# Kernel tuning notes

Hardware: AMD Instinct MI355X
Metric: run time of the kernel (lower is better)

## Reference

```python
import jax, jax.numpy as jnp
import numpy as np

NEG_INF = -1e30  # value the original assigns to exactly-zero scores


def setup_inputs() -> dict:
    key = jax.random.key(0)
    kq, kk, kv = jax.random.split(key, 3)
    B, Lq, Lk, d = 16, 4096, 4096, 64
    queries = jax.random.normal(kq, (B, Lq, d), dtype=jnp.float32)
    keys = jax.random.normal(kk, (B, Lk, d), dtype=jnp.float32)
    values = jax.random.normal(kv, (B, Lk, d), dtype=jnp.float32)
    return {"queries": queries, "keys": keys, "values": values}


def reference(queries, keys, values):
    d = queries.shape[-1]
    # [B, Lq, Lk] full score matrix, scaled
    scores = jnp.einsum("bqd,bkd->bqk", queries, keys) / jnp.sqrt(
        jnp.asarray(d, dtype=queries.dtype)
    )
    # zero-score masking: scores[scores == 0] = -1e30
    scores = jnp.where(scores == 0, jnp.asarray(NEG_INF, dtype=scores.dtype), scores)
    attn = jax.nn.softmax(scores, axis=-1)
    # dropout prob is 0.0 -> identity
    return jnp.einsum("bqk,bkd->bqd", attn, values)
```

## Files before the change

### kernel.cpp

```cpp
#include <hip/hip_runtime.h>
#include <hip/hip_bf16.h>
#include <math.h>

typedef __attribute__((ext_vector_type(4))) float f32x4;
typedef __attribute__((ext_vector_type(8))) short s16x8;

#define B_    16
#define L_    4096
#define D_    64
#define QB    64
#define KVB   64
#define NT    (L_ / KVB)

#define QSCALE 0.18033688011112042f
#define THR    8.0f

__device__ __forceinline__ unsigned short f2bf(float x) {
  union { float f; unsigned u; } v; v.f = x;
  unsigned r = v.u + 0x7FFFu + ((v.u >> 16) & 1u);
  return (unsigned short)(r >> 16);
}

__device__ __forceinline__ int swz(int x) {
  return ((x & 7) ^ ((x >> 3) & 7)) << 4;
}

__device__ __forceinline__ void gload_lds16(const void* g, void* l) {
  __builtin_amdgcn_global_load_lds(
      (const __attribute__((address_space(1))) void*)g,
      (__attribute__((address_space(3))) void*)l, 16, 0, 0);
}

__device__ __forceinline__ unsigned cvtpk_bf16(float lo, float hi) {
  unsigned r;
  asm("v_cvt_pk_bf16_f32 %0, %1, %2" : "=v"(r) : "v"(lo), "v"(hi));
  return r;
}

__device__ __forceinline__ void pl32_swap(unsigned& a, unsigned& b) {
#if __has_builtin(__builtin_amdgcn_permlane32_swap)
  auto r = __builtin_amdgcn_permlane32_swap(a, b, false, false);
  a = r[0]; b = r[1];
#else
  asm volatile("v_permlane32_swap_b32 %0, %1" : "+v"(a), "+v"(b));
#endif
}

__device__ __forceinline__ void pl16_swap(unsigned& a, unsigned& b) {
#if __has_builtin(__builtin_amdgcn_permlane16_swap)
  auto r = __builtin_amdgcn_permlane16_swap(a, b, false, false);
  a = r[0]; b = r[1];
#else
  asm volatile("v_permlane16_swap_b32 %0, %1" : "+v"(a), "+v"(b));
#endif
}

__device__ __forceinline__ float fexp2(float x) {
#if __has_builtin(__builtin_amdgcn_exp2f)
  return __builtin_amdgcn_exp2f(x);
#else
  return exp2f(x);
#endif
}

__global__ __launch_bounds__(256) void prep_kv3(
    const float* __restrict__ Kg, const float* __restrict__ Vg,
    unsigned short* __restrict__ Kw, unsigned short* __restrict__ Vw) {
  const int tid = threadIdx.x;
  int blk = blockIdx.x;
  if (blk < B_ * NT) {
    const float* src = Kg + (size_t)blk * (KVB * D_);
    char* dst = (char*)(Kw + (size_t)blk * (KVB * D_));
#pragma unroll
    for (int c = 0; c < 2; ++c) {
      const int ch  = tid + c * 256;
      const int key = ch >> 3;
      const int seg = ch & 7;
      const float* p = src + key * D_ + seg * 8;
      f32x4 x0 = *(const f32x4*)p;
      f32x4 x1 = *(const f32x4*)(p + 4);
      union { s16x8 v; unsigned w[4]; } t_;
      t_.w[0] = cvtpk_bf16(x0[0], x0[1]);
      t_.w[1] = cvtpk_bf16(x0[2], x0[3]);
      t_.w[2] = cvtpk_bf16(x1[0], x1[1]);
      t_.w[3] = cvtpk_bf16(x1[2], x1[3]);
      *(s16x8*)(dst + ((key * 128 + seg * 16) ^ swz(key))) = t_.v;
    }
  } else {
    blk -= B_ * NT;
    const int skey2 = (tid >> 3) * 2;
    const int sdseg = tid & 7;
    const float* vp0 = Vg + ((size_t)blk * KVB + skey2) * D_ + sdseg * 8;
    char* vout = (char*)(Vw + (size_t)blk * (KVB * D_));
    f32x4 v0 = *(const f32x4*)(vp0);
    f32x4 v1 = *(const f32x4*)(vp0 + 4);
    f32x4 v2 = *(const f32x4*)(vp0 + D_);
    f32x4 v3 = *(const f32x4*)(vp0 + D_ + 4);
#pragma unroll
    for (int u = 0; u < 2; ++u) {
#pragma unroll
      for (int i = 0; i < 4; ++i) {
        const int d = sdseg * 8 + u * 4 + i;
        unsigned pk = cvtpk_bf16(u ? v1[i] : v0[i], u ? v3[i] : v2[i]);
        *(unsigned*)(vout + ((d * 128 + skey2 * 2) ^ swz(d))) = pk;
      }
    }
  }
}

__global__ __launch_bounds__(256) void attn_fwd4(
    const float* __restrict__ Qg, const unsigned short* __restrict__ Kw,
    const unsigned short* __restrict__ Vw, float* __restrict__ Og) {
  __shared__ unsigned short Ks[2][KVB * D_];
  __shared__ unsigned short Vs[2][KVB * D_];

  const int tid  = threadIdx.x;
  const int wv   = tid >> 6;
  const int lane = tid & 63;
  const int rl   = lane & 15;
  const int kb   = lane >> 4;
  const int kb4  = kb * 4;

  const int blk = blockIdx.x;
  const int b   = blk >> 6;
  const int qt  = blk & 63;

  const float* qrow_p = Qg + ((size_t)b * L_ + qt * QB + wv * 16 + rl) * D_;
  s16x8 aq[2];
#pragma unroll
  for (int h = 0; h < 2; ++h) {
    const float* p = qrow_p + h * 32 + kb * 8;
    f32x4 x0 = *(const f32x4*)p;
    f32x4 x1 = *(const f32x4*)(p + 4);
    union { s16x8 v; unsigned w[4]; } t_;
    t_.w[0] = cvtpk_bf16(x0[0] * QSCALE, x0[1] * QSCALE);
    t_.w[1] = cvtpk_bf16(x0[2] * QSCALE, x0[3] * QSCALE);
    t_.w[2] = cvtpk_bf16(x1[0] * QSCALE, x1[1] * QSCALE);
    t_.w[3] = cvtpk_bf16(x1[2] * QSCALE, x1[3] * QSCALE);
    aq[h] = t_.v;
  }

  int koffA[4], koffB[4], voffA[4], voffB[4];
#pragma unroll
  for (int t = 0; t < 4; ++t) {
    const int key = t * 16 + rl;
    const int kbase = key * 128 + kb * 16;
    koffA[t] = kbase ^ swz(key);
    koffB[t] = (kbase + 64) ^ swz(key);
    voffA[t] = kbase ^ swz(key);
    voffB[t] = (kbase + 64) ^ swz(key);
  }

  f32x4 oacc[4];
#pragma unroll
  for (int t = 0; t < 4; ++t) oacc[t] = (f32x4){0.f, 0.f, 0.f, 0.f};
  float m_r = -3.0e38f, l_r = 0.f;

  char* ks0 = (char*)(&Ks[0][0]);
  char* vs0 = (char*)(&Vs[0][0]);
  const int woff = wv * 2048 ;
  const char* kt = (const char*)(Kw + (size_t)b * L_ * D_) + woff + lane * 16;
  const char* vt = (const char*)(Vw + (size_t)b * L_ * D_) + woff + lane * 16;

  auto compute = [&](const char* kbase, const char* vbase) {
    f32x4 s[4];
    __builtin_amdgcn_s_setprio(1);
#pragma unroll
    for (int t = 0; t < 4; ++t) {
      s16x8 k0 = *(const s16x8*)(kbase + koffA[t]);
      s16x8 k1 = *(const s16x8*)(kbase + koffB[t]);
      f32x4 acc = (f32x4){0.f, 0.f, 0.f, 0.f};
      acc = __builtin_amdgcn_mfma_f32_16x16x32_bf16(k0, aq[0], acc, 0, 0, 0);
      acc = __builtin_amdgcn_mfma_f32_16x16x32_bf16(k1, aq[1], acc, 0, 0, 0);
      s[t] = acc;
    }
    __builtin_amdgcn_s_setprio(0);

    float a0 = fmaxf(fmaxf(s[0][0], s[0][1]), s[0][2]);
    float a1 = fmaxf(fmaxf(s[0][3], s[1][0]), s[1][1]);
    float a2 = fmaxf(fmaxf(s[1][2], s[1][3]), s[2][0]);
    float a3 = fmaxf(fmaxf(s[2][1], s[2][2]), s[2][3]);
    float a4 = fmaxf(fmaxf(s[3][0], s[3][1]), s[3][2]);
    float mx = fmaxf(fmaxf(fmaxf(a0, a1), fmaxf(a2, a3)),
                     fmaxf(a4, s[3][3]));

    if (__any(mx > m_r + THR)) {
      float rmx = fmaxf(mx, __shfl_xor(mx, 16));
      rmx = fmaxf(rmx, __shfl_xor(rmx, 32));
      const float mn = fmaxf(m_r, rmx);
      const float alpha = fexp2(m_r - mn);
      m_r = mn;
      l_r *= alpha;
      const float b0 = __shfl(alpha, kb4 + 0);
      const float b1 = __shfl(alpha, kb4 + 1);
      const float b2 = __shfl(alpha, kb4 + 2);
      const float b3 = __shfl(alpha, kb4 + 3);
#pragma unroll
      for (int t = 0; t < 4; ++t) {
        oacc[t][0] *= b0; oacc[t][1] *= b1;
        oacc[t][2] *= b2; oacc[t][3] *= b3;
      }
    }

    unsigned Wp[4][2];
    float rs = 0.f;
#pragma unroll
    for (int t = 0; t < 4; ++t) {
      const float e0 = fexp2(s[t][0] - m_r);
      const float e1 = fexp2(s[t][1] - m_r);
      const float e2 = fexp2(s[t][2] - m_r);
      const float e3 = fexp2(s[t][3] - m_r);
      rs += (e0 + e1) + (e2 + e3);
      Wp[t][0] = cvtpk_bf16(e0, e1);
      Wp[t][1] = cvtpk_bf16(e2, e3);
    }
    l_r += rs;

    union { s16x8 v; unsigned w[4]; } AF0, AF1;
    {
      unsigned x = Wp[0][0], y = Wp[1][0];
      pl32_swap(x, y); pl16_swap(x, y);
      AF0.w[0] = x; AF0.w[2] = y;
    }
    {
      unsigned x = Wp[0][1], y = Wp[1][1];
      pl32_swap(x, y); pl16_swap(x, y);
      AF0.w[1] = x; AF0.w[3] = y;
    }
    {
      unsigned x = Wp[2][0], y = Wp[3][0];
      pl32_swap(x, y); pl16_swap(x, y);
      AF1.w[0] = x; AF1.w[2] = y;
    }
    {
      unsigned x = Wp[2][1], y = Wp[3][1];
      pl32_swap(x, y); pl16_swap(x, y);
      AF1.w[1] = x; AF1.w[3] = y;
    }

    __builtin_amdgcn_s_setprio(1);
#pragma unroll
    for (int t = 0; t < 4; ++t) {
      s16x8 bv0 = *(const s16x8*)(vbase + voffA[t]);
      s16x8 bv1 = *(const s16x8*)(vbase + voffB[t]);
      f32x4 acc = oacc[t];
      acc = __builtin_amdgcn_mfma_f32_16x16x32_bf16(AF0.v, bv0, acc, 0, 0, 0);
      acc = __builtin_amdgcn_mfma_f32_16x16x32_bf16(AF1.v, bv1, acc, 0, 0, 0);
      oacc[t] = acc;
    }
    __builtin_amdgcn_s_setprio(0);
  };

  gload_lds16(kt,        ks0 + woff);
  gload_lds16(kt + 1024, ks0 + woff + 1024);
  gload_lds16(vt,        vs0 + woff);
  gload_lds16(vt + 1024, vs0 + woff + 1024);
  kt += 8192; vt += 8192;
  __syncthreads();

  int boff = 0;
  for (int kv = 0; kv < NT - 1; ++kv) {
    const int nb = boff ^ 8192;
    gload_lds16(kt,        ks0 + nb + woff);
    gload_lds16(kt + 1024, ks0 + nb + woff + 1024);
    gload_lds16(vt,        vs0 + nb + woff);
    gload_lds16(vt + 1024, vs0 + nb + woff + 1024);
    kt += 8192; vt += 8192;

    compute(ks0 + boff, vs0 + boff);
    __syncthreads();
    boff = nb;
  }
  compute(ks0 + boff, vs0 + boff);

  float lt = l_r + __shfl_xor(l_r, 16);
  lt += __shfl_xor(lt, 32);
  const float linv = 1.0f / lt;
  const float i0 = __shfl(linv, kb4 + 0);
  const float i1 = __shfl(linv, kb4 + 1);
  const float i2 = __shfl(linv, kb4 + 2);
  const float i3 = __shfl(linv, kb4 + 3);
  float inv[4] = {i0, i1, i2, i3};

  float* op = Og + ((size_t)b * L_ + qt * QB + wv * 16 + kb4) * D_;
#pragma unroll
  for (int j = 0; j < 4; ++j)
#pragma unroll
    for (int t = 0; t < 4; ++t)
      op[(size_t)j * D_ + t * 16 + rl] = oacc[t][j] * inv[j];
}

__global__ __launch_bounds__(256) void attn_fwd_fb(
    const float* __restrict__ Qg, const float* __restrict__ Kg,
    const float* __restrict__ Vg, float* __restrict__ Og) {
  __shared__ unsigned short Ksf[KVB * D_];
  __shared__ unsigned short Vsf[KVB * D_];
  __shared__ unsigned short Psf[4][16 * KVB];

  const int tid  = threadIdx.x;
  const int wv   = tid >> 6;
  const int lane = tid & 63;
  const int rl   = lane & 15;
  const int kb   = lane >> 4;

  const int blk = blockIdx.x;
  const int b   = blk / (L_ / QB);
  const int qt  = blk % (L_ / QB);

  const float* qrow_p = Qg + ((size_t)b * L_ + qt * QB + wv * 16 + rl) * D_;
  s16x8 aq[2];
#pragma unroll
  for (int h = 0; h < 2; ++h) {
    const float* p = qrow_p + h * 32 + kb * 8;
    f32x4 x0 = *(const f32x4*)p;
    f32x4 x1 = *(const f32x4*)(p + 4);
    s16x8 w;
#pragma unroll
    for (int i = 0; i < 4; ++i) {
      w[i]     = (short)f2bf(x0[i] * QSCALE);
      w[i + 4] = (short)f2bf(x1[i] * QSCALE);
    }
    aq[h] = w;
  }

  f32x4 oacc[4];
  float m_r[4], l_r[4];
#pragma unroll
  for (int t = 0; t < 4; ++t) oacc[t] = (f32x4){0.f, 0.f, 0.f, 0.f};
#pragma unroll
  for (int j = 0; j < 4; ++j) { m_r[j] = -3.0e38f; l_r[j] = 0.f; }

  const float* kb_p = Kg + (size_t)b * L_ * D_;
  const float* vb_p = Vg + (size_t)b * L_ * D_;
  const int skey2 = (tid >> 3) * 2;
  const int sdseg = tid & 7;

  char* ksc = (char*)Ksf;
  char* vsc = (char*)Vsf;
  char* psc = (char*)(Psf[wv]);

  for (int kv = 0; kv < L_; kv += KVB) {
    __syncthreads();
    {
      const float* kp0 = kb_p + (size_t)(kv + skey2) * D_ + sdseg * 8;
      const float* vp0 = vb_p + (size_t)(kv + skey2) * D_ + sdseg * 8;
#pragma unroll
      for (int q2 = 0; q2 < 2; ++q2) {
        const int key = skey2 + q2;
        f32x4 a0 = *(const f32x4*)(kp0 + q2 * D_);
        f32x4 a1 = *(const f32x4*)(kp0 + q2 * D_ + 4);
        s16x8 w;
#pragma unroll
        for (int i = 0; i < 4; ++i) {
          w[i]     = (short)f2bf(a0[i]);
          w[i + 4] = (short)f2bf(a1[i]);
        }
        *(s16x8*)(ksc + ((key * 128 + sdseg * 16) ^ swz(key))) = w;
      }
      f32x4 v0 = *(const f32x4*)(vp0);
      f32x4 v1 = *(const f32x4*)(vp0 + 4);
      f32x4 v2 = *(const f32x4*)(vp0 + D_);
      f32x4 v3 = *(const f32x4*)(vp0 + D_ + 4);
#pragma unroll
      for (int u = 0; u < 2; ++u) {
#pragma unroll
        for (int i = 0; i < 4; ++i) {
          const int d = sdseg * 8 + u * 4 + i;
          unsigned lo = (unsigned)f2bf(u ? v1[i] : v0[i]);
          unsigned hi = (unsigned)f2bf(u ? v3[i] : v2[i]);
          *(unsigned*)(vsc + ((d * 128 + skey2 * 2) ^ swz(d))) = lo | (hi << 16);
        }
      }
    }
    __syncthreads();

    f32x4 s[4];
#pragma unroll
    for (int t = 0; t < 4; ++t) {
      const int key  = t * 16 + rl;
      const int base = key * 128 + kb * 16;
      s16x8 b0 = *(const s16x8*)(ksc + ((base)      ^ swz(key)));
      s16x8 b1 = *(const s16x8*)(ksc + ((base + 64) ^ swz(key)));
      f32x4 acc = (f32x4){0.f, 0.f, 0.f, 0.f};
      acc = __builtin_amdgcn_mfma_f32_16x16x32_bf16(aq[0], b0, acc, 0, 0, 0);
      acc = __builtin_amdgcn_mfma_f32_16x16x32_bf16(aq[1], b1, acc, 0, 0, 0);
      s[t] = acc;
    }

    float alpha[4];
#pragma unroll
    for (int j = 0; j < 4; ++j) {
      float mx = fmaxf(fmaxf(s[0][j], s[1][j]), fmaxf(s[2][j], s[3][j]));
      mx = fmaxf(mx, __shfl_xor(mx, 1));
      mx = fmaxf(mx, __shfl_xor(mx, 2));
      mx = fmaxf(mx, __shfl_xor(mx, 4));
      mx = fmaxf(mx, __shfl_xor(mx, 8));
      const float mn = fmaxf(m_r[j], mx);
      alpha[j] = fexp2(m_r[j] - mn);
      m_r[j]   = mn;
    }

    float rs[4] = {0.f, 0.f, 0.f, 0.f};
#pragma unroll
    for (int t = 0; t < 4; ++t)
#pragma unroll
      for (int j = 0; j < 4; ++j) {
        const float p = fexp2(s[t][j] - m_r[j]);
        rs[j] += p;
        const int row = kb * 4 + j;
        *(unsigned short*)(psc + ((row * 128 + (t * 16 + rl) * 2) ^ swz(row))) = f2bf(p);
      }
#pragma unroll
    for (int j = 0; j < 4; ++j) l_r[j] = l_r[j] * alpha[j] + rs[j];

#pragma unroll
    for (int t = 0; t < 4; ++t)
#pragma unroll
      for (int j = 0; j < 4; ++j) oacc[t][j] *= alpha[j];

    s16x8 ap[2];
#pragma unroll
    for (int h = 0; h < 2; ++h) {
      const int base = rl * 128 + h * 64 + kb * 16;
      ap[h] = *(const s16x8*)(psc + (base ^ swz(rl)));
    }
#pragma unroll
    for (int t = 0; t < 4; ++t) {
      const int d    = t * 16 + rl;
      const int base = d * 128 + kb * 16;
      s16x8 bv0 = *(const s16x8*)(vsc + ((base)      ^ swz(d)));
      s16x8 bv1 = *(const s16x8*)(vsc + ((base + 64) ^ swz(d)));
      f32x4 acc = oacc[t];
      acc = __builtin_amdgcn_mfma_f32_16x16x32_bf16(ap[0], bv0, acc, 0, 0, 0);
      acc = __builtin_amdgcn_mfma_f32_16x16x32_bf16(ap[1], bv1, acc, 0, 0, 0);
      oacc[t] = acc;
    }
  }

  float inv[4];
#pragma unroll
  for (int j = 0; j < 4; ++j) {
    float r = l_r[j];
    r += __shfl_xor(r, 1);
    r += __shfl_xor(r, 2);
    r += __shfl_xor(r, 4);
    r += __shfl_xor(r, 8);
    inv[j] = 1.0f / r;
  }
  float* op = Og + ((size_t)b * L_ + qt * QB + wv * 16 + kb * 4) * D_;
#pragma unroll
  for (int j = 0; j < 4; ++j)
#pragma unroll
    for (int t = 0; t < 4; ++t)
      op[(size_t)j * D_ + t * 16 + rl] = oacc[t][j] * inv[j];
}

extern "C" void kernel_launch(void* const* d_in, const int* in_sizes, int n_in,
                              void* d_out, int out_size, void* d_ws, size_t ws_size,
                              hipStream_t stream) {
  (void)in_sizes; (void)n_in; (void)out_size;
  const float* Q = (const float*)d_in[0];
  const float* K = (const float*)d_in[1];
  const float* V = (const float*)d_in[2];
  float* O = (float*)d_out;

  const size_t need = (size_t)2 * B_ * L_ * D_ * sizeof(unsigned short);
  if (d_ws != nullptr && ws_size >= need) {
    unsigned short* Kw = (unsigned short*)d_ws;
    unsigned short* Vw = Kw + (size_t)B_ * L_ * D_;
    prep_kv3<<<dim3(2 * B_ * NT), 256, 0, stream>>>(K, V, Kw, Vw);
    attn_fwd4<<<dim3(B_ * (L_ / QB)), 256, 0, stream>>>(Q, Kw, Vw, O);
  } else {
    attn_fwd_fb<<<dim3(B_ * (L_ / QB)), 256, 0, stream>>>(Q, K, V, O);
  }
}
```

Measured before the change: 197.0 us.

## Process two 16-row Q subtiles per wave to double K/V reuse per block

```diff
diff --git a/kernel.cpp b/kernel.cpp
--- a/kernel.cpp
+++ b/kernel.cpp
@@ -8,7 +8,7 @@
 #define B_    16
 #define L_    4096
 #define D_    64
-#define QB    64
+#define QB    128
 #define KVB   64
 #define NT    (L_ / KVB)
 
@@ -63,9 +63,10 @@
 #endif
 }
 
-__global__ __launch_bounds__(256) void prep_kv3(
+__global__ __launch_bounds__(256) void prep_kv4(
     const float* __restrict__ Kg, const float* __restrict__ Vg,
     unsigned short* __restrict__ Kw, unsigned short* __restrict__ Vw) {
+  __shared__ unsigned short vim[KVB * D_];
   const int tid = threadIdx.x;
   int blk = blockIdx.x;
   if (blk < B_ * NT) {
@@ -91,7 +92,7 @@
     const int skey2 = (tid >> 3) * 2;
     const int sdseg = tid & 7;
     const float* vp0 = Vg + ((size_t)blk * KVB + skey2) * D_ + sdseg * 8;
-    char* vout = (char*)(Vw + (size_t)blk * (KVB * D_));
+    char* vimc = (char*)vim;
     f32x4 v0 = *(const f32x4*)(vp0);
     f32x4 v1 = *(const f32x4*)(vp0 + 4);
     f32x4 v2 = *(const f32x4*)(vp0 + D_);
@@ -102,13 +103,20 @@
       for (int i = 0; i < 4; ++i) {
         const int d = sdseg * 8 + u * 4 + i;
         unsigned pk = cvtpk_bf16(u ? v1[i] : v0[i], u ? v3[i] : v2[i]);
-        *(unsigned*)(vout + ((d * 128 + skey2 * 2) ^ swz(d))) = pk;
+        *(unsigned*)(vimc + ((d * 128 + skey2 * 2) ^ swz(d))) = pk;
       }
     }
-  }
-}
-
-__global__ __launch_bounds__(256) void attn_fwd4(
+    __syncthreads();
+    char* vout = (char*)(Vw + (size_t)blk * (KVB * D_));
+#pragma unroll
+    for (int c = 0; c < 2; ++c) {
+      const int off = c * 4096 + tid * 16;
+      *(s16x8*)(vout + off) = *(const s16x8*)(vimc + off);
+    }
+  }
+}
+
+__global__ __launch_bounds__(256, 2) void attn_fwd5(
     const float* __restrict__ Qg, const unsigned short* __restrict__ Kw,
     const unsigned short* __restrict__ Vw, float* __restrict__ Og) {
   __shared__ unsigned short Ks[2][KVB * D_];
@@ -122,131 +130,152 @@
   const int kb4  = kb * 4;
 
   const int blk = blockIdx.x;
-  const int b   = blk >> 6;
-  const int qt  = blk & 63;
-
-  const float* qrow_p = Qg + ((size_t)b * L_ + qt * QB + wv * 16 + rl) * D_;
-  s16x8 aq[2];
-#pragma unroll
-  for (int h = 0; h < 2; ++h) {
-    const float* p = qrow_p + h * 32 + kb * 8;
-    f32x4 x0 = *(const f32x4*)p;
-    f32x4 x1 = *(const f32x4*)(p + 4);
-    union { s16x8 v; unsigned w[4]; } t_;
-    t_.w[0] = cvtpk_bf16(x0[0] * QSCALE, x0[1] * QSCALE);
-    t_.w[1] = cvtpk_bf16(x0[2] * QSCALE, x0[3] * QSCALE);
-    t_.w[2] = cvtpk_bf16(x1[0] * QSCALE, x1[1] * QSCALE);
-    t_.w[3] = cvtpk_bf16(x1[2] * QSCALE, x1[3] * QSCALE);
-    aq[h] = t_.v;
-  }
-
-  int koffA[4], koffB[4], voffA[4], voffB[4];
+  const int b   = blk >> 5;
+  const int qt  = blk & 31;
+
+  const float* qbase = Qg + ((size_t)b * L_ + qt * QB + wv * 32) * D_;
+  s16x8 aq0[2], aq1[2];
+#pragma unroll
+  for (int qh = 0; qh < 2; ++qh) {
+    const float* qrow_p = qbase + (qh * 16 + rl) * D_;
+#pragma unroll
+    for (int h = 0; h < 2; ++h) {
+      const float* p = qrow_p + h * 32 + kb * 8;
+      f32x4 x0 = *(const f32x4*)p;
+      f32x4 x1 = *(const f32x4*)(p + 4);
+      union { s16x8 v; unsigned w[4]; } t_;
+      t_.w[0] = cvtpk_bf16(x0[0] * QSCALE, x0[1] * QSCALE);
+      t_.w[1] = cvtpk_bf16(x0[2] * QSCALE, x0[3] * QSCALE);
+      t_.w[2] = cvtpk_bf16(x1[0] * QSCALE, x1[1] * QSCALE);
+      t_.w[3] = cvtpk_bf16(x1[2] * QSCALE, x1[3] * QSCALE);
+      if (qh == 0) aq0[h] = t_.v; else aq1[h] = t_.v;
+    }
+  }
+
+  int offA[4], offB[4];
 #pragma unroll
   for (int t = 0; t < 4; ++t) {
-    const int key = t * 16 + rl;
-    const int kbase = key * 128 + kb * 16;
-    koffA[t] = kbase ^ swz(key);
-    koffB[t] = (kbase + 64) ^ swz(key);
-    voffA[t] = kbase ^ swz(key);
-    voffB[t] = (kbase + 64) ^ swz(key);
-  }
-
-  f32x4 oacc[4];
-#pragma unroll
-  for (int t = 0; t < 4; ++t) oacc[t] = (f32x4){0.f, 0.f, 0.f, 0.f};
-  float m_r = -3.0e38f, l_r = 0.f;
+    const int row  = t * 16 + rl;
+    const int base = row * 128 + kb * 16;
+    offA[t] = base ^ swz(row);
+    offB[t] = (base + 64) ^ swz(row);
+  }
+
+  f32x4 oacc0[4], oacc1[4];
+#pragma unroll
+  for (int t = 0; t < 4; ++t) {
+    oacc0[t] = (f32x4){0.f, 0.f, 0.f, 0.f};
+    oacc1[t] = (f32x4){0.f, 0.f, 0.f, 0.f};
+  }
+  float m0 = -3.0e38f, m1 = -3.0e38f, l0 = 0.f, l1 = 0.f;
 
   char* ks0 = (char*)(&Ks[0][0]);
   char* vs0 = (char*)(&Vs[0][0]);
-  const int woff = wv * 2048 ;
+  const int woff = wv * 2048;
   const char* kt = (const char*)(Kw + (size_t)b * L_ * D_) + woff + lane * 16;
   const char* vt = (const char*)(Vw + (size_t)b * L_ * D_) + woff + lane * 16;
 
   auto compute = [&](const char* kbase, const char* vbase) {
-    f32x4 s[4];
+    f32x4 s0[4], s1[4];
     __builtin_amdgcn_s_setprio(1);
 #pragma unroll
     for (int t = 0; t < 4; ++t) {
-      s16x8 k0 = *(const s16x8*)(kbase + koffA[t]);
-      s16x8 k1 = *(const s16x8*)(kbase + koffB[t]);
-      f32x4 acc = (f32x4){0.f, 0.f, 0.f, 0.f};
-      acc = __builtin_amdgcn_mfma_f32_16x16x32_bf16(k0, aq[0], acc, 0, 0, 0);
-      acc = __builtin_amdgcn_mfma_f32_16x16x32_bf16(k1, aq[1], acc, 0, 0, 0);
-      s[t] = acc;
+      s16x8 k0 = *(const s16x8*)(kbase + offA[t]);
+      s16x8 k1 = *(const s16x8*)(kbase + offB[t]);
+      f32x4 a = (f32x4){0.f, 0.f, 0.f, 0.f};
+      f32x4 c = (f32x4){0.f, 0.f, 0.f, 0.f};
+      a = __builtin_amdgcn_mfma_f32_16x16x32_bf16(k0, aq0[0], a, 0, 0, 0);
+      c = __builtin_amdgcn_mfma_f32_16x16x32_bf16(k0, aq1[0], c, 0, 0, 0);
+      a = __builtin_amdgcn_mfma_f32_16x16x32_bf16(k1, aq0[1], a, 0, 0, 0);
+      c = __builtin_amdgcn_mfma_f32_16x16x32_bf16(k1, aq1[1], c, 0, 0, 0);
+      s0[t] = a; s1[t] = c;
     }
     __builtin_amdgcn_s_setprio(0);
 
-    float a0 = fmaxf(fmaxf(s[0][0], s[0][1]), s[0][2]);
-    float a1 = fmaxf(fmaxf(s[0][3], s[1][0]), s[1][1]);
-    float a2 = fmaxf(fmaxf(s[1][2], s[1][3]), s[2][0]);
-    float a3 = fmaxf(fmaxf(s[2][1], s[2][2]), s[2][3]);
-    float a4 = fmaxf(fmaxf(s[3][0], s[3][1]), s[3][2]);
-    float mx = fmaxf(fmaxf(fmaxf(a0, a1), fmaxf(a2, a3)),
-                     fmaxf(a4, s[3][3]));
-
-    if (__any(mx > m_r + THR)) {
-      float rmx = fmaxf(mx, __shfl_xor(mx, 16));
-      rmx = fmaxf(rmx, __shfl_xor(rmx, 32));
-      const float mn = fmaxf(m_r, rmx);
-      const float alpha = fexp2(m_r - mn);
-      m_r = mn;
-      l_r *= alpha;
-      const float b0 = __shfl(alpha, kb4 + 0);
-      const float b1 = __shfl(alpha, kb4 + 1);
-      const float b2 = __shfl(alpha, kb4 + 2);
-      const float b3 = __shfl(alpha, kb4 + 3);
-#pragma unroll
-      for (int t = 0; t < 4; ++t) {
-        oacc[t][0] *= b0; oacc[t][1] *= b1;
-        oacc[t][2] *= b2; oacc[t][3] *= b3;
+    float x0 = fmaxf(fmaxf(s0[0][0], s0[0][1]), fmaxf(s0[0][2], s0[0][3]));
+    float x1 = fmaxf(fmaxf(s0[1][0], s0[1][1]), fmaxf(s0[1][2], s0[1][3]));
+    float x2 = fmaxf(fmaxf(s0[2][0], s0[2][1]), fmaxf(s0[2][2], s0[2][3]));
+    float x3 = fmaxf(fmaxf(s0[3][0], s0[3][1]), fmaxf(s0[3][2], s0[3][3]));
+    float mx0 = fmaxf(fmaxf(x0, x1), fmaxf(x2, x3));
+    float y0 = fmaxf(fmaxf(s1[0][0], s1[0][1]), fmaxf(s1[0][2], s1[0][3]));
+    float y1 = fmaxf(fmaxf(s1[1][0], s1[1][1]), fmaxf(s1[1][2], s1[1][3]));
+    float y2 = fmaxf(fmaxf(s1[2][0], s1[2][1]), fmaxf(s1[2][2], s1[2][3]));
+    float y3 = fmaxf(fmaxf(s1[3][0], s1[3][1]), fmaxf(s1[3][2], s1[3][3]));
+    float mx1 = fmaxf(fmaxf(y0, y1), fmaxf(y2, y3));
+
+    if (__any((mx0 > m0 + THR) || (mx1 > m1 + THR))) {
+      float r0 = fmaxf(mx0, __shfl_xor(mx0, 16));
+      r0 = fmaxf(r0, __shfl_xor(r0, 32));
+      float r1 = fmaxf(mx1, __shfl_xor(mx1, 16));
+      r1 = fmaxf(r1, __shfl_xor(r1, 32));
+      const float n0 = fmaxf(m0, r0);
+      const float n1 = fmaxf(m1, r1);
+      const float al0 = fexp2(m0 - n0);
+      const float al1 = fexp2(m1 - n1);
+      m0 = n0; m1 = n1;
+      l0 *= al0; l1 *= al1;
+#pragma unroll
+      for (int j = 0; j < 4; ++j) {
+        const float b0 = __shfl(al0, kb4 + j);
+        const float b1 = __shfl(al1, kb4 + j);
+#pragma unroll
+        for (int t = 0; t < 4; ++t) {
+          oacc0[t][j] *= b0;
+          oacc1[t][j] *= b1;
+        }
       }
     }
 
-    unsigned Wp[4][2];
-    float rs = 0.f;
+    unsigned W0[4][2], W1[4][2];
+    float rs0 = 0.f, rs1 = 0.f;
 #pragma unroll
     for (int t = 0; t < 4; ++t) {
-      const float e0 = fexp2(s[t][0] - m_r);
-      const float e1 = fexp2(s[t][1] - m_r);
-      const float e2 = fexp2(s[t][2] - m_r);
-      const float e3 = fexp2(s[t][3] - m_r);
-      rs += (e0 + e1) + (e2 + e3);
-      Wp[t][0] = cvtpk_bf16(e0, e1);
-      Wp[t][1] = cvtpk_bf16(e2, e3);
-    }
-    l_r += rs;
-
-    union { s16x8 v; unsigned w[4]; } AF0, AF1;
-    {
-      unsigned x = Wp[0][0], y = Wp[1][0];
-      pl32_swap(x, y); pl16_swap(x, y);
-      AF0.w[0] = x; AF0.w[2] = y;
-    }
-    {
-      unsigned x = Wp[0][1], y = Wp[1][1];
-      pl32_swap(x, y); pl16_swap(x, y);
-      AF0.w[1] = x; AF0.w[3] = y;
-    }
-    {
-      unsigned x = Wp[2][0], y = Wp[3][0];
-      pl32_swap(x, y); pl16_swap(x, y);
-      AF1.w[0] = x; AF1.w[2] = y;
-    }
-    {
-      unsigned x = Wp[2][1], y = Wp[3][1];
-      pl32_swap(x, y); pl16_swap(x, y);
-      AF1.w[1] = x; AF1.w[3] = y;
+      const float e0 = fexp2(s0[t][0] - m0);
+      const float e1 = fexp2(s0[t][1] - m0);
+      const float e2 = fexp2(s0[t][2] - m0);
+      const float e3 = fexp2(s0[t][3] - m0);
+      rs0 += (e0 + e1) + (e2 + e3);
+      W0[t][0] = cvtpk_bf16(e0, e1);
+      W0[t][1] = cvtpk_bf16(e2, e3);
+      const float f0 = fexp2(s1[t][0] - m1);
+      const float f1 = fexp2(s1[t][1] - m1);
+      const float f2 = fexp2(s1[t][2] - m1);
+      const float f3 = fexp2(s1[t][3] - m1);
+      rs1 += (f0 + f1) + (f2 + f3);
+      W1[t][0] = cvtpk_bf16(f0, f1);
+      W1[t][1] = cvtpk_bf16(f2, f3);
+    }
+    l0 += rs0; l1 += rs1;
+
+    union { s16x8 v; unsigned w[4]; } A00, A01, A10, A11;
+#pragma unroll
+    for (int u = 0; u < 2; ++u) {
+      { unsigned x = W0[0][u], y = W0[1][u];
+        pl32_swap(x, y); pl16_swap(x, y);
+        A00.w[u] = x; A00.w[u + 2] = y; }
+      { unsigned x = W0[2][u], y = W0[3][u];
+        pl32_swap(x, y); pl16_swap(x, y);
+        A01.w[u] = x; A01.w[u + 2] = y; }
+      { unsigned x = W1[0][u], y = W1[1][u];
+        pl32_swap(x, y); pl16_swap(x, y);
+        A10.w[u] = x; A10.w[u + 2] = y; }
+      { unsigned x = W1[2][u], y = W1[3][u];
+        pl32_swap(x, y); pl16_swap(x, y);
+        A11.w[u] = x; A11.w[u + 2] = y; }
     }
 
     __builtin_amdgcn_s_setprio(1);
 #pragma unroll
     for (int t = 0; t < 4; ++t) {
-      s16x8 bv0 = *(const s16x8*)(vbase + voffA[t]);
-      s16x8 bv1 = *(const s16x8*)(vbase + voffB[t]);
-      f32x4 acc = oacc[t];
-      acc = __builtin_amdgcn_mfma_f32_16x16x32_bf16(AF0.v, bv0, acc, 0, 0, 0);
-      acc = __builtin_amdgcn_mfma_f32_16x16x32_bf16(AF1.v, bv1, acc, 0, 0, 0);
-      oacc[t] = acc;
+      s16x8 bv0 = *(const s16x8*)(vbase + offA[t]);
+      s16x8 bv1 = *(const s16x8*)(vbase + offB[t]);
+      f32x4 a = oacc0[t];
+      f32x4 c = oacc1[t];
+      a = __builtin_amdgcn_mfma_f32_16x16x32_bf16(A00.v, bv0, a, 0, 0, 0);
+      c = __builtin_amdgcn_mfma_f32_16x16x32_bf16(A10.v, bv0, c, 0, 0, 0);
+      a = __builtin_amdgcn_mfma_f32_16x16x32_bf16(A01.v, bv1, a, 0, 0, 0);
+      c = __builtin_amdgcn_mfma_f32_16x16x32_bf16(A11.v, bv1, c, 0, 0, 0);
+      oacc0[t] = a; oacc1[t] = c;
     }
     __builtin_amdgcn_s_setprio(0);
   };
@@ -273,21 +302,26 @@
   }
   compute(ks0 + boff, vs0 + boff);
 
-  float lt = l_r + __shfl_xor(l_r, 16);
-  lt += __shfl_xor(lt, 32);
-  const float linv = 1.0f / lt;
-  const float i0 = __shfl(linv, kb4 + 0);
-  const float i1 = __shfl(linv, kb4 + 1);
-  const float i2 = __shfl(linv, kb4 + 2);
-  const float i3 = __shfl(linv, kb4 + 3);
-  float inv[4] = {i0, i1, i2, i3};
-
-  float* op = Og + ((size_t)b * L_ + qt * QB + wv * 16 + kb4) * D_;
-#pragma unroll
-  for (int j = 0; j < 4; ++j)
-#pragma unroll
-    for (int t = 0; t < 4; ++t)
-      op[(size_t)j * D_ + t * 16 + rl] = oacc[t][j] * inv[j];
+  float t0 = l0 + __shfl_xor(l0, 16);
+  t0 += __shfl_xor(t0, 32);
+  float t1 = l1 + __shfl_xor(l1, 16);
+  t1 += __shfl_xor(t1, 32);
+  const float v0i = 1.0f / t0;
+  const float v1i = 1.0f / t1;
+
+  float* ob = Og + ((size_t)b * L_ + qt * QB + wv * 32 + kb4) * D_;
+#pragma unroll
+  for (int j = 0; j < 4; ++j) {
+    const float i0 = __shfl(v0i, kb4 + j);
+    const float i1 = __shfl(v1i, kb4 + j);
+    float* r0 = ob + (size_t)j * D_;
+    float* r1 = r0 + 16 * D_;
+#pragma unroll
+    for (int t = 0; t < 4; ++t) {
+      r0[t * 16 + rl] = oacc0[t][j] * i0;
+      r1[t * 16 + rl] = oacc1[t][j] * i1;
+    }
+  }
 }
 
 __global__ __launch_bounds__(256) void attn_fwd_fb(
@@ -304,10 +338,10 @@
   const int kb   = lane >> 4;
 
   const int blk = blockIdx.x;
-  const int b   = blk / (L_ / QB);
-  const int qt  = blk % (L_ / QB);
-
-  const float* qrow_p = Qg + ((size_t)b * L_ + qt * QB + wv * 16 + rl) * D_;
+  const int b   = blk / (L_ / 64);
+  const int qt  = blk % (L_ / 64);
+
+  const float* qrow_p = Qg + ((size_t)b * L_ + qt * 64 + wv * 16 + rl) * D_;
   s16x8 aq[2];
 #pragma unroll
   for (int h = 0; h < 2; ++h) {
@@ -447,7 +481,7 @@
     r += __shfl_xor(r, 8);
     inv[j] = 1.0f / r;
   }
-  float* op = Og + ((size_t)b * L_ + qt * QB + wv * 16 + kb * 4) * D_;
+  float* op = Og + ((size_t)b * L_ + qt * 64 + wv * 16 + kb * 4) * D_;
 #pragma unroll
   for (int j = 0; j < 4; ++j)
 #pragma unroll
@@ -468,9 +502,9 @@
   if (d_ws != nullptr && ws_size >= need) {
     unsigned short* Kw = (unsigned short*)d_ws;
     unsigned short* Vw = Kw + (size_t)B_ * L_ * D_;
-    prep_kv3<<<dim3(2 * B_ * NT), 256, 0, stream>>>(K, V, Kw, Vw);
-    attn_fwd4<<<dim3(B_ * (L_ / QB)), 256, 0, stream>>>(Q, Kw, Vw, O);
+    prep_kv4<<<dim3(2 * B_ * NT), 256, 0, stream>>>(K, V, Kw, Vw);
+    attn_fwd5<<<dim3(B_ * (L_ / QB)), 256, 0, stream>>>(Q, Kw, Vw, O);
   } else {
-    attn_fwd_fb<<<dim3(B_ * (L_ / QB)), 256, 0, stream>>>(Q, K, V, O);
-  }
-}
+    attn_fwd_fb<<<dim3(B_ * (L_ / 64)), 256, 0, stream>>>(Q, K, V, O);
+  }
+}
```

Measured after the change: 193.5 us. No clear change (-1.8%).
